# Performance work log

Hardware: AMD Instinct MI355X
Metric: run time of the kernel (lower is better)

The kernel has to match this reference:

```python
import jax, jax.numpy as jnp
import numpy as np

B = 65536          # number of graphs
NPG = 28           # nodes per graph (896 = 32*28)
N = B * NPG
K = 4              # random within-graph neighbors per node


def setup_inputs() -> dict:
    key = jax.random.key(0)
    ks = jax.random.split(key, 8)
    x = jax.random.normal(ks[0], (N, 2), dtype=jnp.float32)
    # within-graph random edges: each node i -> K random targets in its graph
    local = jax.random.randint(ks[1], (N, K), 0, NPG)
    base = (jnp.arange(N, dtype=jnp.int32) // NPG) * NPG
    dst = (base[:, None] + local.astype(jnp.int32)).reshape(-1)
    src = jnp.repeat(jnp.arange(N, dtype=jnp.int32), K)
    edge_index = jnp.stack([src, dst])  # [2, E]
    conv_w = jax.random.normal(ks[2], (2, 32), dtype=jnp.float32) * (1.0 / np.sqrt(2))
    conv_b = jax.random.normal(ks[3], (32,), dtype=jnp.float32) * 0.01
    fc1_w = jax.random.normal(ks[4], (896, 256), dtype=jnp.float32) * (1.0 / np.sqrt(896))
    fc1_b = jax.random.normal(ks[5], (256,), dtype=jnp.float32) * 0.01
    fc2_w = jax.random.normal(ks[6], (256, 2), dtype=jnp.float32) * (1.0 / np.sqrt(256))
    fc2_b = jax.random.normal(ks[7], (2,), dtype=jnp.float32) * 0.01
    return {"x": x, "edge_index": edge_index, "conv_w": conv_w, "conv_b": conv_b,
            "fc1_w": fc1_w, "fc1_b": fc1_b, "fc2_w": fc2_w, "fc2_b": fc2_b}


def gcn_conv(x, edge_index, w, b):
    n = x.shape[0]
    h = x @ w  # [N, 32]
    loops = jnp.arange(n, dtype=edge_index.dtype)
    src = jnp.concatenate([edge_index[0], loops])
    dst = jnp.concatenate([edge_index[1], loops])
    deg = jax.ops.segment_sum(jnp.ones_like(dst, dtype=h.dtype), dst, num_segments=n)
    dinv = jnp.where(deg > 0, jax.lax.rsqrt(jnp.maximum(deg, 1.0)), 0.0)
    norm = dinv[src] * dinv[dst]  # [E']
    agg = jax.ops.segment_sum(h[src] * norm[:, None], dst, num_segments=n)
    return agg + b


def reference(x, edge_index, conv_w, conv_b, fc1_w, fc1_b, fc2_w, fc2_b):
    h = jax.nn.relu(gcn_conv(x, edge_index, conv_w, conv_b))  # [N, 32]
    h = h.reshape(-1, 896)                                    # [B, 896]
    h = h @ fc1_w + fc1_b                                     # [B, 256]
    nrm = jnp.sqrt(jnp.sum(h * h, axis=1, keepdims=True))
    hn = h / jnp.maximum(nrm, 1e-12)                          # F.normalize(dim=1)
    x1 = hn @ fc2_w + fc2_b                                   # [B, 2]
    mu = jax.nn.sigmoid(x1[:, 0])
    theta = jax.nn.softplus(x1[:, 1])
    return hn, mu, theta
```

## Files before the change

### kernel.cpp

```cpp
#include <hip/hip_runtime.h>
#include <hip/hip_bf16.h>
#include <stdint.h>

#define NPG 28
#define KDIM 896
#define NOUT 256
#define BM 128
#define BK 32
#define KT (KDIM / BK)

typedef __attribute__((ext_vector_type(8))) __bf16 bf16x8;
typedef __attribute__((ext_vector_type(8))) ushort us8;
typedef __attribute__((ext_vector_type(4))) float f32x4;

__device__ __forceinline__ ushort f2bf(float v) {
    uint u = __float_as_uint(v);
    return (ushort)((u + 0x7fffu + ((u >> 16) & 1u)) >> 16);
}

__device__ __forceinline__ void gload_lds16(const void* g, void* l) {
    __builtin_amdgcn_global_load_lds(
        (const __attribute__((address_space(1))) void*)(uintptr_t)g,
        (__attribute__((address_space(3))) void*)(uintptr_t)l,
        16, 0, 0);
}

__global__ __launch_bounds__(256) void k_agg(
    const float* __restrict__ x, const int* __restrict__ dst,
    const float* __restrict__ f1w,
    float* __restrict__ acc2g, ushort* __restrict__ wt, int nAgg)
{
    __shared__ int   pk[8][32];
    __shared__ float sx[8][32][2];
    __shared__ float t[32][33];

    const int tid = threadIdx.x;

    if ((int)blockIdx.x >= nAgg) {
        int b = blockIdx.x - nAgg;
        int n0 = (b & 7) * 32, k0 = (b >> 3) * 32;
        int tx = tid & 31, ty = tid >> 5;
#pragma unroll
        for (int q = 0; q < 4; ++q)
            t[ty + q * 8][tx] = f1w[(k0 + ty + q * 8) * NOUT + n0 + tx];
        __syncthreads();
#pragma unroll
        for (int q = 0; q < 4; ++q)
            wt[(long)(k0 >> 5) * (NOUT * BK) + (n0 + ty + q * 8) * BK + tx] =
                f2bf(t[tx][ty + q * 8]);
        return;
    }

    const int g = tid >> 5;
    const int j = tid & 31;
    const long gb = ((long)blockIdx.x * 8 + g) * NPG;

    float2 xx = make_float2(0.f, 0.f);
    if (j < NPG) {
        int4 d4 = ((const int4*)dst)[gb + j];
        xx = ((const float2*)x)[gb + j];
        int gbi = (int)gb;
        pk[g][j] = (d4.x - gbi) | ((d4.y - gbi) << 8) |
                   ((d4.z - gbi) << 16) | ((d4.w - gbi) << 24);
    }
    __syncthreads();

    const uint repj = (uint)j * 0x01010101u;
    uint cp0 = 0, cp1 = 0, cp2 = 0, cp3 = 0;
    int cnt = 0;
#pragma unroll
    for (int s4 = 0; s4 < 7; ++s4) {
        int4 pv = *(const int4*)&pk[g][s4 * 4];
#pragma unroll
        for (int r = 0; r < 4; ++r) {
            uint v = ((const uint*)&pv)[r] ^ repj;
            uint zb = ~(((v & 0x7F7F7F7Fu) + 0x7F7F7F7Fu) | v) & 0x80808080u;
            uint c = (uint)__popc(zb);
            cnt += (int)c;
            int s = s4 * 4 + r;
            uint nib = c << ((s & 7) * 4);
            if (s < 8)       cp0 |= nib;
            else if (s < 16) cp1 |= nib;
            else if (s < 24) cp2 |= nib;
            else             cp3 |= nib;
        }
    }

    const float dinv = rsqrtf((float)(1 + cnt));
    const float sx0 = xx.x * dinv, sx1 = xx.y * dinv;
    if (j < NPG) {
        sx[g][j][0] = sx0;
        sx[g][j][1] = sx1;
    }
    __syncthreads();

    float a0 = sx0, a1 = sx1;
#pragma unroll
    for (int s = 0; s < NPG; ++s) {
        float2 sv = *(const float2*)&sx[g][s][0];
        uint cpw = (s < 8) ? cp0 : (s < 16) ? cp1 : (s < 24) ? cp2 : cp3;
        float cf = (float)((cpw >> ((s & 7) * 4)) & 0xFu);
        a0 += cf * sv.x;
        a1 += cf * sv.y;
    }

    if (j < NPG) {
        const long Btot = (long)nAgg * 8;
        const long graph = (long)blockIdx.x * 8 + g;
        ((float2*)acc2g)[(long)j * Btot + graph] = make_float2(a0 * dinv, a1 * dinv);
    }
}

__device__ __forceinline__ void stage_b2(const char* WtB, ushort* BsX, int kt, int tid) {
    const int o = (tid & 3) ^ ((tid >> 3) & 3);
    const long tb = (long)kt * 16384 + (tid >> 2) * 64 + o * 16;
    gload_lds16(WtB + tb,        (char*)BsX + tid * 16);
    gload_lds16(WtB + tb + 8192, (char*)BsX + 8192 + tid * 16);
}

__device__ __forceinline__ void agen_write(ushort* AsX, float2 av, int awoff,
                                           const float* w0, const float* w1, const float* bb) {
    union { us8 v; uint u[4]; } pk;
#pragma unroll
    for (int k = 0; k < 4; ++k) {
        float e0 = fmaxf(av.x * w0[2 * k]     + av.y * w1[2 * k]     + bb[2 * k],     0.f);
        float e1 = fmaxf(av.x * w0[2 * k + 1] + av.y * w1[2 * k + 1] + bb[2 * k + 1], 0.f);
        __hip_bfloat162 h = __float22bfloat162_rn(make_float2(e0, e1));
        pk.u[k] = *reinterpret_cast<uint*>(&h);
    }
    *(us8*)&AsX[awoff] = pk.v;
}

__device__ __forceinline__ void compute_mfma(const ushort* AsX, const ushort* BsX,
                                             f32x4 acc[4][4], int a_off, int b_off) {
    bf16x8 bfr[4], afr[4];
#pragma unroll
    for (int ni = 0; ni < 4; ++ni)
        bfr[ni] = *(const bf16x8*)(&BsX[b_off + ni * 512]);
#pragma unroll
    for (int mi = 0; mi < 4; ++mi)
        afr[mi] = *(const bf16x8*)(&AsX[a_off + mi * 512]);
    __builtin_amdgcn_s_setprio(1);
#pragma unroll
    for (int mi = 0; mi < 4; ++mi)
#pragma unroll
        for (int ni = 0; ni < 4; ++ni)
            acc[mi][ni] = __builtin_amdgcn_mfma_f32_16x16x32_bf16(
                afr[mi], bfr[ni], acc[mi][ni], 0, 0, 0);
    __builtin_amdgcn_s_setprio(0);
}

__global__ __launch_bounds__(512, 3) void k_gemm(
    const float* __restrict__ acc2g, const ushort* __restrict__ Wt,
    const float* __restrict__ cw, const float* __restrict__ cb,
    const float* __restrict__ f1b, const float* __restrict__ f2w,
    const float* __restrict__ f2b, float* __restrict__ out, int Bsz)
{
    __shared__ ushort As0[BM * BK], As1[BM * BK];
    __shared__ ushort Bs0[NOUT * BK], Bs1[NOUT * BK];

    const int tid = threadIdx.x;
    const int w = tid >> 6, l = tid & 63;
    const int wM = w >> 2, wN = w & 3;
    const int l15 = l & 15, lhi = (l >> 4) & 3;
    const long m0 = (long)blockIdx.x * BM;
    const long Btot = Bsz;

    const int ao = __builtin_amdgcn_readfirstlane(w & 3);
    const int arow = (w >> 2) * 64 + l;
    const int awoff = arow * 32 + ((ao ^ ((l >> 1) & 3)) * 8);
    float w0[8], w1[8], bb[8];
#pragma unroll
    for (int k = 0; k < 8; ++k) {
        w0[k] = cw[ao * 8 + k]; w1[k] = cw[32 + ao * 8 + k]; bb[k] = cb[ao * 8 + k];
    }

    const int swz = (lhi ^ ((l15 >> 1) & 3)) * 8;
    const int a_off = (wM * 64 + l15) * 32 + swz;
    const int b_off = (wN * 64 + l15) * 32 + swz;

    const float2* a2 = (const float2*)acc2g;
    const char* WtB = (const char*)Wt;
    const long ag = m0 + arow;

    f32x4 acc[4][4];
#pragma unroll
    for (int mi = 0; mi < 4; ++mi)
#pragma unroll
        for (int ni = 0; ni < 4; ++ni) acc[mi][ni] = (f32x4){0.f, 0.f, 0.f, 0.f};

    {
        float2 av0 = a2[ag];
        stage_b2(WtB, Bs0, 0, tid);
        agen_write(As0, av0, awoff, w0, w1, bb);
    }
    float2 avn = a2[Btot + ag];
    __syncthreads();

    for (int kt = 0; kt < KT; kt += 2) {
        stage_b2(WtB, Bs1, kt + 1, tid);
        float2 avn2 = (kt + 2 < KT) ? a2[(long)(kt + 2) * Btot + ag] : make_float2(0.f, 0.f);
        agen_write(As1, avn, awoff, w0, w1, bb);
        compute_mfma(As0, Bs0, acc, a_off, b_off);
        __syncthreads();

        if (kt + 2 < KT) {
            stage_b2(WtB, Bs0, kt + 2, tid);
            avn = a2[(long)(kt + 3) * Btot + ag];
            agen_write(As0, avn2, awoff, w0, w1, bb);
        }
        compute_mfma(As1, Bs1, acc, a_off, b_off);
        __syncthreads();
    }

    float b1[4], w20[4], w21[4];
#pragma unroll
    for (int ni = 0; ni < 4; ++ni) {
        int col = wN * 64 + ni * 16 + l15;
        b1[ni] = f1b[col];
        w20[ni] = f2w[col * 2 + 0];
        w21[ni] = f2w[col * 2 + 1];
    }
    float* red    = (float*)As0;
    float* red_ss = red;
    float* red_p0 = red + 512;
    float* red_p1 = red + 1024;
    float* red_rn = red + 1536;

#pragma unroll
    for (int mi = 0; mi < 4; ++mi) {
        float ssr[4], p0r[4], p1r[4];
#pragma unroll
        for (int r = 0; r < 4; ++r) { ssr[r] = 0.f; p0r[r] = 0.f; p1r[r] = 0.f; }
#pragma unroll
        for (int ni = 0; ni < 4; ++ni) {
#pragma unroll
            for (int r = 0; r < 4; ++r) {
                float v = acc[mi][ni][r] + b1[ni];
                acc[mi][ni][r] = v;
                ssr[r] += v * v;
                p0r[r] += v * w20[ni];
                p1r[r] += v * w21[ni];
            }
        }
#pragma unroll
        for (int m = 1; m < 16; m <<= 1) {
#pragma unroll
            for (int r = 0; r < 4; ++r) {
                ssr[r] += __shfl_xor(ssr[r], m);
                p0r[r] += __shfl_xor(p0r[r], m);
                p1r[r] += __shfl_xor(p1r[r], m);
            }
        }
        if (l15 == 0) {
            int rowb = wM * 64 + mi * 16 + lhi * 4;
#pragma unroll
            for (int r = 0; r < 4; ++r) {
                red_ss[(rowb + r) * 4 + wN] = ssr[r];
                red_p0[(rowb + r) * 4 + wN] = p0r[r];
                red_p1[(rowb + r) * 4 + wN] = p1r[r];
            }
        }
    }
    __syncthreads();

    if (tid < BM) {
        int row = tid;
        float ss = red_ss[row * 4 + 0] + red_ss[row * 4 + 1] + red_ss[row * 4 + 2] + red_ss[row * 4 + 3];
        float p0 = red_p0[row * 4 + 0] + red_p0[row * 4 + 1] + red_p0[row * 4 + 2] + red_p0[row * 4 + 3];
        float p1 = red_p1[row * 4 + 0] + red_p1[row * 4 + 1] + red_p1[row * 4 + 2] + red_p1[row * 4 + 3];
        float rn = 1.0f / fmaxf(sqrtf(ss), 1e-12f);
        float x0 = p0 * rn + f2b[0];
        float x1 = p1 * rn + f2b[1];
        float mu = 1.0f / (1.0f + expf(-x0));
        float th = (x1 > 0.f) ? (x1 + log1pf(expf(-x1))) : log1pf(expf(x1));
        long gr = m0 + row;
        out[(long)Bsz * NOUT + gr] = mu;
        out[(long)Bsz * NOUT + Bsz + gr] = th;
        red_rn[row] = rn;
    }
    __syncthreads();

#pragma unroll
    for (int mi = 0; mi < 4; ++mi) {
        float rn[4];
#pragma unroll
        for (int r = 0; r < 4; ++r) rn[r] = red_rn[wM * 64 + mi * 16 + lhi * 4 + r];
#pragma unroll
        for (int ni = 0; ni < 4; ++ni) {
#pragma unroll
            for (int r = 0; r < 4; ++r) {
                long row = m0 + wM * 64 + mi * 16 + lhi * 4 + r;
                out[row * NOUT + wN * 64 + ni * 16 + l15] = acc[mi][ni][r] * rn[r];
            }
        }
    }
}

extern "C" void kernel_launch(void* const* d_in, const int* in_sizes, int n_in,
                              void* d_out, int out_size, void* d_ws, size_t ws_size,
                              hipStream_t stream) {
    const float* x   = (const float*)d_in[0];
    const int*   ei  = (const int*)d_in[1];
    const float* cw  = (const float*)d_in[2];
    const float* cb  = (const float*)d_in[3];
    const float* f1w = (const float*)d_in[4];
    const float* f1b = (const float*)d_in[5];
    const float* f2w = (const float*)d_in[6];
    const float* f2b = (const float*)d_in[7];
    float* out = (float*)d_out;

    const int Nn  = in_sizes[0] / 2;
    const int Bsz = Nn / NPG;
    const int E   = in_sizes[1] / 2;
    const int* dst = ei + E;

    float*  acc2g = (float*)d_ws;
    ushort* Wt    = (ushort*)(acc2g + (size_t)Nn * 2);

    const int nAgg = Bsz / 8;
    const int nTr  = (KDIM / 32) * (NOUT / 32);

    k_agg<<<nAgg + nTr, 256, 0, stream>>>(x, dst, f1w, acc2g, Wt, nAgg);
    k_gemm<<<Bsz / BM, 512, 0, stream>>>(acc2g, Wt, cw, cb, f1b, f2w, f2b, out, Bsz);
}
```

Baseline: 67.58 us.

## Triple-buffer B tiles and stream A inputs via LDS ring with async loads

Replaces the double-buffered GEMM main loop with a three-stage B buffer and a three-slot LDS ring for the per-node aggregated inputs. Those inputs are now fetched with direct global-to-LDS loads instead of register loads. Explicit vmcnt/lgkmcnt waits and raw barriers replace __syncthreads, so there is one barrier per k-step. The aim is to keep two tiles of loads in flight while MFMA runs and to hide global latency. In exchange it adds LDS use, which may reduce occupancy, and hand-counted waitcnts that are fragile if stage_b2's load count changes.

```diff
diff --git a/kernel.cpp b/kernel.cpp
--- a/kernel.cpp
+++ b/kernel.cpp
@@ -157,14 +157,15 @@
     const float* __restrict__ f2b, float* __restrict__ out, int Bsz)
 {
     __shared__ ushort As0[BM * BK], As1[BM * BK];
-    __shared__ ushort Bs0[NOUT * BK], Bs1[NOUT * BK];
+    __shared__ ushort Bs0[NOUT * BK], Bs1[NOUT * BK], Bs2[NOUT * BK];
+    __shared__ float2 Aring[3][8][64];
 
     const int tid = threadIdx.x;
     const int w = tid >> 6, l = tid & 63;
     const int wM = w >> 2, wN = w & 3;
     const int l15 = l & 15, lhi = (l >> 4) & 3;
     const long m0 = (long)blockIdx.x * BM;
-    const long Btot = Bsz;
+    const long BszB = (long)Bsz * 8;
 
     const int ao = __builtin_amdgcn_readfirstlane(w & 3);
     const int arow = (w >> 2) * 64 + l;
@@ -179,9 +180,9 @@
     const int a_off = (wM * 64 + l15) * 32 + swz;
     const int b_off = (wN * 64 + l15) * 32 + swz;
 
-    const float2* a2 = (const float2*)acc2g;
+    const char* A2B = (const char*)acc2g;
     const char* WtB = (const char*)Wt;
-    const long ag = m0 + arow;
+    const long agbase = (m0 + (long)(w >> 2) * 64 + 2 * l) * 8;
 
     f32x4 acc[4][4];
 #pragma unroll
@@ -189,29 +190,50 @@
 #pragma unroll
         for (int ni = 0; ni < 4; ++ni) acc[mi][ni] = (f32x4){0.f, 0.f, 0.f, 0.f};
 
+    stage_b2(WtB, Bs0, 0, tid);
+    if (l < 32) gload_lds16(A2B + agbase,        (char*)&Aring[0][w][0]);
+    stage_b2(WtB, Bs1, 1, tid);
+    if (l < 32) gload_lds16(A2B + BszB + agbase, (char*)&Aring[1][w][0]);
+    asm volatile("s_waitcnt vmcnt(3)" ::: "memory");
+    __builtin_amdgcn_s_barrier();
+    agen_write(As0, Aring[0][w][l], awoff, w0, w1, bb);
+    asm volatile("s_waitcnt lgkmcnt(0)" ::: "memory");
+    __builtin_amdgcn_s_barrier();
+
+#define PH(BC, BS, AC, AN, RR, RS, KS) do {                                    \
+        stage_b2(WtB, BS, (KS), tid);                                          \
+        if (l < 32) gload_lds16(A2B + (long)(KS) * BszB + agbase,              \
+                                (char*)&Aring[RS][w][0]);                      \
+        compute_mfma(AC, BC, acc, a_off, b_off);                               \
+        asm volatile("s_waitcnt vmcnt(3)" ::: "memory");                       \
+        agen_write(AN, Aring[RR][w][l], awoff, w0, w1, bb);                    \
+        asm volatile("s_waitcnt lgkmcnt(0)" ::: "memory");                     \
+        __builtin_amdgcn_s_barrier();                                          \
+    } while (0)
+
+    for (int kt = 0; kt < 24; kt += 6) {
+        PH(Bs0, Bs2, As0, As1, 1, 2, kt + 2);
+        PH(Bs1, Bs0, As1, As0, 2, 0, kt + 3);
+        PH(Bs2, Bs1, As0, As1, 0, 1, kt + 4);
+        PH(Bs0, Bs2, As1, As0, 1, 2, kt + 5);
+        PH(Bs1, Bs0, As0, As1, 2, 0, kt + 6);
+        PH(Bs2, Bs1, As1, As0, 0, 1, kt + 7);
+    }
+    PH(Bs0, Bs2, As0, As1, 1, 2, 26);
+    PH(Bs1, Bs0, As1, As0, 2, 0, 27);
     {
-        float2 av0 = a2[ag];
-        stage_b2(WtB, Bs0, 0, tid);
-        agen_write(As0, av0, awoff, w0, w1, bb);
-    }
-    float2 avn = a2[Btot + ag];
-    __syncthreads();
-
-    for (int kt = 0; kt < KT; kt += 2) {
-        stage_b2(WtB, Bs1, kt + 1, tid);
-        float2 avn2 = (kt + 2 < KT) ? a2[(long)(kt + 2) * Btot + ag] : make_float2(0.f, 0.f);
-        agen_write(As1, avn, awoff, w0, w1, bb);
-        compute_mfma(As0, Bs0, acc, a_off, b_off);
-        __syncthreads();
-
-        if (kt + 2 < KT) {
-            stage_b2(WtB, Bs0, kt + 2, tid);
-            avn = a2[(long)(kt + 3) * Btot + ag];
-            agen_write(As0, avn2, awoff, w0, w1, bb);
-        }
-        compute_mfma(As1, Bs1, acc, a_off, b_off);
-        __syncthreads();
-    }
+        compute_mfma(As0, Bs2, acc, a_off, b_off);
+        asm volatile("s_waitcnt vmcnt(0)" ::: "memory");
+        agen_write(As1, Aring[0][w][l], awoff, w0, w1, bb);
+        asm volatile("s_waitcnt lgkmcnt(0)" ::: "memory");
+        __builtin_amdgcn_s_barrier();
+    }
+    {
+        compute_mfma(As1, Bs0, acc, a_off, b_off);
+        asm volatile("s_waitcnt lgkmcnt(0)" ::: "memory");
+        __builtin_amdgcn_s_barrier();
+    }
+#undef PH
 
     float b1[4], w20[4], w21[4];
 #pragma unroll
```

Measured after the change: 76.65 us. +13.4%, slower.
